# Kernel tuning notes

Measured on AMD Instinct MI355X. Metric: run time of the kernel, lower is better.

Reference implementation:

```python
import jax, jax.numpy as jnp
import numpy as np

HEIGHT, WIDTH, NUM_FRAMES, DIM = 64, 64, 16, 1280
GRIDS = [(8, 32, 32), (16, 16, 16), (4, 48, 48), (1, 64, 64)]  # ragged (t,h,w) per sample


def _sincos_1d(embed_dim, t_size):
    # matches get_1d_sincos_pos_embed_from_grid
    omega = np.arange(embed_dim // 2, dtype=np.float32) / (embed_dim / 2.0)
    omega = 1.0 / (10000.0 ** omega)
    pos = np.arange(t_size, dtype=np.float32)
    out = np.einsum('m,d->md', pos, omega)
    return np.concatenate([np.sin(out), np.cos(out)], axis=1).astype(np.float32)  # [t, dim]


def setup_inputs() -> dict:
    key = jax.random.key(0)
    k1, k2 = jax.random.split(key)
    total_tokens = sum(t * h * w for t, h, w in GRIDS)  # 25600
    x = jax.random.normal(k1, (total_tokens, DIM), dtype=jnp.float32)
    weight = jax.random.normal(k2, (HEIGHT, WIDTH, DIM), dtype=jnp.float32)  # learnable 2D pos emb
    time_weight = jnp.asarray(_sincos_1d(DIM, NUM_FRAMES))  # [num_frames, dim] sincos buffer
    grid_thws = np.asarray(GRIDS, dtype=np.int64)  # static per-sample (t,h,w)
    return {"x": x, "weight": weight, "time_weight": time_weight, "grid_thws": grid_thws}


def reference(x, weight, time_weight, grid_thws):
    H, W, D = weight.shape
    grids = np.asarray(grid_thws).tolist()  # static metadata; loop is over ragged samples
    pos_embs = []
    for t, h, w in grids:
        if (h, w) == (H, W):
            pe2d = weight.reshape(-1, D)  # [h*w, D]
        else:
            # torch path: fp32 bicubic interpolation of [H,W,D] -> [h,w,D]
            pe2d = jax.image.resize(weight.astype(jnp.float32), (h, w, D),
                                    method='bicubic').astype(x.dtype).reshape(-1, D)
        if t == 1:
            pe3d = pe2d
        else:
            # broadcast-add temporal sincos embedding: [t,1,D] + [1,h*w,D]
            pe3d = (pe2d[None, :, :] + time_weight[:t, None, :]).reshape(-1, D)
        pos_embs.append(pe3d)
    return x + jnp.concatenate(pos_embs, axis=0)
```

## Files before the change

kernel.cpp:

```cpp
#include <hip/hip_runtime.h>


__device__ __forceinline__ float keys_cubic(float x) {
    x = fabsf(x);
    if (x >= 2.0f) return 0.0f;
    if (x >= 1.0f) return ((-0.5f * x + 2.5f) * x - 4.0f) * x + 2.0f;
    return ((1.5f * x - 2.5f) * x) * x + 1.0f;
}

__device__ __forceinline__ void tap_params(int o, int out_size,
                                           int& i0, int& n, float& sf,
                                           float& inv_ks, float& inv_sum) {
    float inv_scale = 64.0f / (float)out_size;
    float ks = inv_scale;
    float radius = 2.0f * ks;
    sf = ((float)o + 0.5f) * inv_scale - 0.5f;
    int lo = (int)ceilf(sf - radius); if (lo < 0) lo = 0;
    int hi = (int)floorf(sf + radius); if (hi > 63) hi = 63;
    n = hi - lo + 1;
    i0 = lo;
    inv_ks = 1.0f / ks;
    float sum = 0.0f;
    for (int k = 0; k < n; ++k)
        sum += keys_cubic((sf - (float)(lo + k)) * inv_ks);
    inv_sum = 1.0f / sum;
}

#define TMP_STRIDE 68
#define PE_STRIDE  68
#define MAXTAP 17

__global__ __launch_bounds__(256) void fused_pe_kernel(const float* __restrict__ x,
                                                       const float* __restrict__ weight,
                                                       const float* __restrict__ tw,
                                                       float* __restrict__ out) {
    __shared__ float tmp[64 * TMP_STRIDE];
    __shared__ float pe_lds[48 * PE_STRIDE];
    __shared__ float vcoef[MAXTAP];
    __shared__ int   vmeta[2];
    __shared__ float hcoef[48][MAXTAP + 1];
    __shared__ int   hj0[48];
    __shared__ int   hn[48];

    int td  = blockIdx.x % 20;
    int row = blockIdx.x / 20;
    int d0  = td * 64;
    int tid = threadIdx.x;

    if (row >= 96) {
        int oy = row - 96;
        const float* wrow = weight + (size_t)oy * 64 * 1280 + d0;
        size_t obase = (size_t)(21504 + oy * 64) * 1280 + d0;
        for (int item = tid; item < 1024; item += 256) {
            int ox = item >> 4, f4 = item & 15;
            size_t xo = obase + (size_t)ox * 1280 + (f4 << 2);
            float4 xv = *(const float4*)(x + xo);
            float4 pv = *(const float4*)(wrow + (size_t)ox * 1280 + (f4 << 2));
            float4 o = make_float4(xv.x + pv.x, xv.y + pv.y, xv.z + pv.z, xv.w + pv.w);
            *(float4*)(out + xo) = o;
        }
    } else {
        int out_h, out_w, oy, t, tok_off, hw;
        if (row < 32)      { out_h = 32; out_w = 32; oy = row;      t = 8;  tok_off = 0;     hw = 1024; }
        else if (row < 48) { out_h = 16; out_w = 16; oy = row - 32; t = 16; tok_off = 8192;  hw = 256;  }
        else               { out_h = 48; out_w = 48; oy = row - 48; t = 4;  tok_off = 12288; hw = 2304; }

        if (tid == 192) {
            int i0, n; float sf, ik, is;
            tap_params(oy, out_h, i0, n, sf, ik, is);
            vmeta[0] = i0; vmeta[1] = n;
            for (int k = 0; k < n; ++k)
                vcoef[k] = keys_cubic((sf - (float)(i0 + k)) * ik) * is;
        }
        if (tid < out_w) {
            int j0, n; float sf, ik, is;
            tap_params(tid, out_w, j0, n, sf, ik, is);
            hj0[tid] = j0; hn[tid] = n;
            for (int k = 0; k < n; ++k)
                hcoef[tid][k] = keys_cubic((sf - (float)(j0 + k)) * ik) * is;
        }
        __syncthreads();

        int i0 = vmeta[0], nh = vmeta[1];
        for (int item = tid; item < 1024; item += 256) {
            int sx = item >> 4;
            int f4 = item & 15;
            const float* src = weight + (size_t)sx * 1280 + d0 + (f4 << 2);
            float4 acc = make_float4(0.f, 0.f, 0.f, 0.f);
            for (int k = 0; k < nh; ++k) {
                float c = vcoef[k];
                float4 v = *(const float4*)(src + (size_t)(i0 + k) * (64 * 1280));
                acc.x += c * v.x; acc.y += c * v.y; acc.z += c * v.z; acc.w += c * v.w;
            }
            *(float4*)&tmp[sx * TMP_STRIDE + (f4 << 2)] = acc;
        }
        __syncthreads();

        for (int item = tid; item < (out_w << 4); item += 256) {
            int ox = item >> 4;
            int f4 = item & 15;
            int j0 = hj0[ox], nw = hn[ox];
            float4 acc = make_float4(0.f, 0.f, 0.f, 0.f);
            for (int k = 0; k < nw; ++k) {
                float c = hcoef[ox][k];
                float4 v = *(const float4*)&tmp[(j0 + k) * TMP_STRIDE + (f4 << 2)];
                acc.x += c * v.x; acc.y += c * v.y; acc.z += c * v.z; acc.w += c * v.w;
            }
            *(float4*)&pe_lds[ox * PE_STRIDE + (f4 << 2)] = acc;
        }
        __syncthreads();

        size_t rbase = (size_t)(tok_off + oy * out_w) * 1280 + d0;
        int nitems = out_w << 4;
        for (int f = 0; f < t; ++f) {
            size_t fbase = rbase + (size_t)f * hw * 1280;
            const float* twf = tw + (size_t)f * 1280 + d0;
            for (int item = tid; item < nitems; item += 256) {
                int ox = item >> 4;
                int f4 = item & 15;
                size_t xo = fbase + (size_t)ox * 1280 + (f4 << 2);
                float4 xv = *(const float4*)(x + xo);
                float4 pv = *(const float4*)&pe_lds[ox * PE_STRIDE + (f4 << 2)];
                float4 tv = *(const float4*)(twf + (f4 << 2));
                float4 o = make_float4(xv.x + pv.x + tv.x, xv.y + pv.y + tv.y,
                                       xv.z + pv.z + tv.z, xv.w + pv.w + tv.w);
                *(float4*)(out + xo) = o;
            }
        }
    }
}

extern "C" void kernel_launch(void* const* d_in, const int* in_sizes, int n_in,
                              void* d_out, int out_size, void* d_ws, size_t ws_size,
                              hipStream_t stream) {
    const float* x      = (const float*)d_in[0];
    const float* weight = (const float*)d_in[1];
    const float* tw     = (const float*)d_in[2];
    float* out = (float*)d_out;

    hipLaunchKernelGGL(fused_pe_kernel, dim3(3200), dim3(256), 0, stream,
                       x, weight, tw, out);
}
```

Measured before the change: 262.9 us.

## Split feature dim into 32-wide tiles and flatten frame loop across threads

Halves the per-block feature slice from 64 to 32 columns, doubling the grid to 6400 blocks and shrinking LDS so more blocks fit per CU (launch bounds now request 8 blocks). The per-frame output loop is flattened so all 256 threads stay busy across frames even when a row has fewer than 256 items (e.g. 16-wide grids). The cost is that the vertical resize pass re-reads more weight rows and recomputes tap coefficients in twice as many blocks. The horizontal coefficient table is also packed with a per-grid stride.

```diff
diff --git a/kernel.cpp b/kernel.cpp
--- a/kernel.cpp
+++ b/kernel.cpp
@@ -26,33 +26,34 @@
     inv_sum = 1.0f / sum;
 }
 
-#define TMP_STRIDE 68
-#define PE_STRIDE  68
+#define NDT 40
+#define TMP_STRIDE 36
+#define PE_STRIDE  36
 #define MAXTAP 17
 
-__global__ __launch_bounds__(256) void fused_pe_kernel(const float* __restrict__ x,
-                                                       const float* __restrict__ weight,
-                                                       const float* __restrict__ tw,
-                                                       float* __restrict__ out) {
+__global__ __launch_bounds__(256, 8) void fused_pe_kernel(const float* __restrict__ x,
+                                                          const float* __restrict__ weight,
+                                                          const float* __restrict__ tw,
+                                                          float* __restrict__ out) {
     __shared__ float tmp[64 * TMP_STRIDE];
     __shared__ float pe_lds[48 * PE_STRIDE];
     __shared__ float vcoef[MAXTAP];
     __shared__ int   vmeta[2];
-    __shared__ float hcoef[48][MAXTAP + 1];
+    __shared__ float hcoef[336];
     __shared__ int   hj0[48];
     __shared__ int   hn[48];
 
-    int td  = blockIdx.x % 20;
-    int row = blockIdx.x / 20;
-    int d0  = td * 64;
+    int td  = blockIdx.x % NDT;
+    int row = blockIdx.x / NDT;
+    int d0  = td * 32;
     int tid = threadIdx.x;
 
     if (row >= 96) {
         int oy = row - 96;
         const float* wrow = weight + (size_t)oy * 64 * 1280 + d0;
         size_t obase = (size_t)(21504 + oy * 64) * 1280 + d0;
-        for (int item = tid; item < 1024; item += 256) {
-            int ox = item >> 4, f4 = item & 15;
+        for (int item = tid; item < 512; item += 256) {
+            int ox = item >> 3, f4 = item & 7;
             size_t xo = obase + (size_t)ox * 1280 + (f4 << 2);
             float4 xv = *(const float4*)(x + xo);
             float4 pv = *(const float4*)(wrow + (size_t)ox * 1280 + (f4 << 2));
@@ -60,10 +61,10 @@
             *(float4*)(out + xo) = o;
         }
     } else {
-        int out_h, out_w, oy, t, tok_off, hw;
-        if (row < 32)      { out_h = 32; out_w = 32; oy = row;      t = 8;  tok_off = 0;     hw = 1024; }
-        else if (row < 48) { out_h = 16; out_w = 16; oy = row - 32; t = 16; tok_off = 8192;  hw = 256;  }
-        else               { out_h = 48; out_w = 48; oy = row - 48; t = 4;  tok_off = 12288; hw = 2304; }
+        int out_h, out_w, oy, t, tok_off, hw, hs;
+        if (row < 32)      { out_h = 32; out_w = 32; oy = row;      t = 8;  tok_off = 0;     hw = 1024; hs = 10; }
+        else if (row < 48) { out_h = 16; out_w = 16; oy = row - 32; t = 16; tok_off = 8192;  hw = 256;  hs = 18; }
+        else               { out_h = 48; out_w = 48; oy = row - 48; t = 4;  tok_off = 12288; hw = 2304; hs = 7;  }
 
         if (tid == 192) {
             int i0, n; float sf, ik, is;
@@ -77,14 +78,14 @@
             tap_params(tid, out_w, j0, n, sf, ik, is);
             hj0[tid] = j0; hn[tid] = n;
             for (int k = 0; k < n; ++k)
-                hcoef[tid][k] = keys_cubic((sf - (float)(j0 + k)) * ik) * is;
+                hcoef[tid * hs + k] = keys_cubic((sf - (float)(j0 + k)) * ik) * is;
         }
         __syncthreads();
 
         int i0 = vmeta[0], nh = vmeta[1];
-        for (int item = tid; item < 1024; item += 256) {
-            int sx = item >> 4;
-            int f4 = item & 15;
+        for (int item = tid; item < 512; item += 256) {
+            int sx = item >> 3;
+            int f4 = item & 7;
             const float* src = weight + (size_t)sx * 1280 + d0 + (f4 << 2);
             float4 acc = make_float4(0.f, 0.f, 0.f, 0.f);
             for (int k = 0; k < nh; ++k) {
@@ -96,13 +97,15 @@
         }
         __syncthreads();
 
-        for (int item = tid; item < (out_w << 4); item += 256) {
-            int ox = item >> 4;
-            int f4 = item & 15;
+        int nitems = out_w << 3;
+        for (int item = tid; item < nitems; item += 256) {
+            int ox = item >> 3;
+            int f4 = item & 7;
             int j0 = hj0[ox], nw = hn[ox];
+            const float* hc = &hcoef[ox * hs];
             float4 acc = make_float4(0.f, 0.f, 0.f, 0.f);
             for (int k = 0; k < nw; ++k) {
-                float c = hcoef[ox][k];
+                float c = hc[k];
                 float4 v = *(const float4*)&tmp[(j0 + k) * TMP_STRIDE + (f4 << 2)];
                 acc.x += c * v.x; acc.y += c * v.y; acc.z += c * v.z; acc.w += c * v.w;
             }
@@ -111,21 +114,20 @@
         __syncthreads();
 
         size_t rbase = (size_t)(tok_off + oy * out_w) * 1280 + d0;
-        int nitems = out_w << 4;
-        for (int f = 0; f < t; ++f) {
-            size_t fbase = rbase + (size_t)f * hw * 1280;
-            const float* twf = tw + (size_t)f * 1280 + d0;
-            for (int item = tid; item < nitems; item += 256) {
-                int ox = item >> 4;
-                int f4 = item & 15;
-                size_t xo = fbase + (size_t)ox * 1280 + (f4 << 2);
-                float4 xv = *(const float4*)(x + xo);
-                float4 pv = *(const float4*)&pe_lds[ox * PE_STRIDE + (f4 << 2)];
-                float4 tv = *(const float4*)(twf + (f4 << 2));
-                float4 o = make_float4(xv.x + pv.x + tv.x, xv.y + pv.y + tv.y,
-                                       xv.z + pv.z + tv.z, xv.w + pv.w + tv.w);
-                *(float4*)(out + xo) = o;
-            }
+        int f = 0, it = tid;
+        if (it >= nitems) { it -= nitems; f = 1; }
+        while (f < t) {
+            int ox = it >> 3, f4 = it & 7;
+            size_t xo = rbase + (size_t)f * hw * 1280 + (size_t)ox * 1280 + (f4 << 2);
+            float4 xv = *(const float4*)(x + xo);
+            float4 pv = *(const float4*)&pe_lds[ox * PE_STRIDE + (f4 << 2)];
+            float4 tv = *(const float4*)(tw + (size_t)f * 1280 + d0 + (f4 << 2));
+            float4 o = make_float4(xv.x + pv.x + tv.x, xv.y + pv.y + tv.y,
+                                   xv.z + pv.z + tv.z, xv.w + pv.w + tv.w);
+            *(float4*)(out + xo) = o;
+            it += 256;
+            if (it >= nitems) { it -= nitems; ++f; }
+            if (it >= nitems) { it -= nitems; ++f; }
         }
     }
 }
@@ -138,6 +140,6 @@
     const float* tw     = (const float*)d_in[2];
     float* out = (float*)d_out;
 
-    hipLaunchKernelGGL(fused_pe_kernel, dim3(3200), dim3(256), 0, stream,
+    hipLaunchKernelGGL(fused_pe_kernel, dim3(160 * NDT), dim3(256), 0, stream,
                        x, weight, tw, out);
 }
```

Result: slower. 275.3 us (+4.7%).
